# Optimization experiments

Hardware: AMD Instinct MI355X
Metric: run time of the kernel (lower is better)

## Reference

```python
import jax, jax.numpy as jnp
from jax import lax
import numpy as np

D_MODEL = 96; D_STATE = 16; SSM_RATIO = 2.0; D_CONV = 3; K = 4
D_INNER = int(SSM_RATIO * D_MODEL)      # 192
DT_RANK = -(-D_MODEL // 16)             # ceil(96/16) = 6
B_SZ = 4; H = 32; W = 32

# ---- zig-zag (snake) index helpers (static numpy) ----
def _snake_h(Hh, Ww):
    idx = np.tile(np.arange(Ww), (Hh, 1)); idx[1::2] = idx[1::2, ::-1]; return idx  # (H,W)

def _snake_v(Hh, Ww):
    idx = np.tile(np.arange(Hh)[:, None], (1, Ww)); idx[:, 1::2] = idx[::-1, 1::2]; return idx  # (H,W)

def _h_scan(x, d):
    Hh, Ww = x.shape[-2:]
    if d == 'left':
        x = jnp.flip(x, (-1, -2))
    return x[:, :, np.arange(Hh)[:, None], _snake_h(Hh, Ww)]

def _v_scan(x, d):
    Bb, Cc, Hh, Ww = x.shape
    if d == 'up':
        x = jnp.flip(x, (-1, -2))
    t = x[:, :, _snake_v(Hh, Ww), np.arange(Ww)[None, :]]  # gather along H per column
    return jnp.swapaxes(t, -1, -2).reshape(Bb, Cc, Hh, Ww)

def _h_merge(x, d):
    Hh, Ww = x.shape[-2:]
    t = x[:, :, np.arange(Hh)[:, None], _snake_h(Hh, Ww)]
    if d == 'left':
        t = jnp.flip(t, (-1, -2))
    return t

def _v_merge(x, d):
    Hh, Ww = x.shape[-2:]
    t2 = jnp.swapaxes(x, -1, -2)  # (B,C,W,H); requires H==W like the torch source
    t = t2[:, :, _snake_v(Hh, Ww), np.arange(Ww)[None, :]]
    if d == 'up':
        t = jnp.flip(t, (-1, -2))
    return t

def cross_scan(x):
    return jnp.stack([_v_scan(x, 'down'), _v_scan(x, 'up'), _h_scan(x, 'right'), _h_scan(x, 'left')], axis=1)

def cross_merge(ys):
    return (_v_merge(ys[:, 0], 'down') + _v_merge(ys[:, 1], 'up')
            + _h_merge(ys[:, 2], 'right') + _h_merge(ys[:, 3], 'left'))

def selective_scan(u, delta, A, Bs, Cs, Dp, delta_bias):
    # u,delta:(B,K,D,L)  A:(K,D,N)  Bs,Cs:(B,K,N,L)  Dp,delta_bias:(K,D)
    delta = jax.nn.softplus(delta + delta_bias[None, :, :, None])
    dA = jnp.exp(jnp.einsum('bkdl,kdn->lbkdn', delta, A))
    dBu = jnp.einsum('bkdl,bkdl,bknl->lbkdn', delta, u, Bs)
    Ct = jnp.moveaxis(Cs, -1, 0)  # (L,B,K,N)
    def step(h, inp):
        dA_t, dBu_t, c_t = inp
        h = dA_t * h + dBu_t
        return h, jnp.einsum('bkdn,bkn->bkd', h, c_t)
    h0 = jnp.zeros(dA.shape[1:], u.dtype)
    _, ys = lax.scan(step, h0, (dA, dBu, Ct))
    return jnp.moveaxis(ys, 0, -1) + Dp[None, :, :, None] * u  # (B,K,D,L)

def setup_inputs() -> dict:
    key = jax.random.key(0)
    ks = jax.random.split(key, 8)
    x = jax.random.normal(ks[0], (B_SZ, D_MODEL, H, W), jnp.float32)
    in_proj_w = jax.random.normal(ks[1], (2 * D_INNER, D_MODEL), jnp.float32) * (D_MODEL ** -0.5)
    conv_w = jax.random.normal(ks[2], (D_INNER, 1, D_CONV, D_CONV), jnp.float32) * 0.2  # depthwise
    conv_b = jnp.zeros((D_INNER,), jnp.float32)
    x_proj_w = jax.random.normal(ks[3], (K, DT_RANK + 2 * D_STATE, D_INNER), jnp.float32) * (D_INNER ** -0.5)
    s = DT_RANK ** -0.5
    dt_w = jax.random.uniform(ks[4], (K, D_INNER, DT_RANK), jnp.float32, -s, s)
    dt = jax.random.uniform(ks[5], (K, D_INNER), jnp.float32, 0.001, 0.1)
    dt_b = jnp.log(jnp.expm1(dt))  # inverse softplus, as in dt_init
    A_logs = jnp.tile(jnp.log(jnp.arange(1, D_STATE + 1, dtype=jnp.float32)), (K * D_INNER, 1))
    Ds = jnp.ones((K * D_INNER,), jnp.float32)
    gn_gamma = jnp.ones((D_INNER,), jnp.float32)
    gn_beta = jnp.zeros((D_INNER,), jnp.float32)
    out_proj_w = jax.random.normal(ks[6], (D_MODEL, D_INNER), jnp.float32) * (D_INNER ** -0.5)
    return {'x': x, 'in_proj_w': in_proj_w, 'conv_w': conv_w, 'conv_b': conv_b,
            'x_proj_w': x_proj_w, 'dt_w': dt_w, 'dt_b': dt_b, 'A_logs': A_logs, 'Ds': Ds,
            'gn_gamma': gn_gamma, 'gn_beta': gn_beta, 'out_proj_w': out_proj_w}

def reference(x, in_proj_w, conv_w, conv_b, x_proj_w, dt_w, dt_b, A_logs, Ds, gn_gamma, gn_beta, out_proj_w):
    Bb, _, Hh, Ww = x.shape; L = Hh * Ww
    xz = jnp.einsum('bchw,oc->bohw', x, in_proj_w)          # in_proj (1x1 conv, no bias)
    xx, z = jnp.split(xz, 2, axis=1)
    z = jax.nn.silu(z)
    xx = lax.conv_general_dilated(xx, conv_w, (1, 1), 'SAME', feature_group_count=D_INNER,
                                  dimension_numbers=('NCHW', 'OIHW', 'NCHW')) + conv_b[None, :, None, None]
    xx = jax.nn.silu(xx)
    xs = cross_scan(xx).reshape(Bb, K, D_INNER, L)          # 4-direction zig-zag scan
    x_dbl = jnp.einsum('bkdl,kcd->bkcl', xs, x_proj_w)
    dts = jnp.einsum('bkrl,kdr->bkdl', x_dbl[:, :, :DT_RANK], dt_w)
    Bs = x_dbl[:, :, DT_RANK:DT_RANK + D_STATE]
    Cs = x_dbl[:, :, DT_RANK + D_STATE:]
    A = -jnp.exp(A_logs).reshape(K, D_INNER, D_STATE)
    y = selective_scan(xs, dts, A, Bs, Cs, Ds.reshape(K, D_INNER), dt_b)
    y = cross_merge(y.reshape(Bb, K, D_INNER, Hh, Ww))       # (B,D,H,W)
    # out_norm: GroupNorm(1, d_inner) == layernorm over (C,H,W) per sample
    mu = jnp.mean(y, axis=(1, 2, 3), keepdims=True)
    var = jnp.var(y, axis=(1, 2, 3), keepdims=True)
    y = (y - mu) * lax.rsqrt(var + 1e-6)
    y = y * gn_gamma[None, :, None, None] + gn_beta[None, :, None, None]
    y = y * z
    return jnp.einsum('bchw,oc->bohw', y, out_proj_w)
```

## Files before the change

kernel.cpp:

```cpp
#include <hip/hip_runtime.h>
#include <math.h>

#define Bsz 4
#define DM 96
#define DI 192
#define NS 16
#define RK 6
#define KK 4
#define HH 32
#define WW 32
#define LL 1024
#define NC 32
#define CS 32

__device__ __forceinline__ float silu_f(float x) { return x / (1.f + __expf(-x)); }

__device__ __forceinline__ float2 pk_mul(float2 a, float2 b) {
    return make_float2(a.x * b.x, a.y * b.y);
}
__device__ __forceinline__ float2 pk_fma(float2 a, float2 b, float2 c) {
    return make_float2(fmaf(a.x, b.x, c.x), fmaf(a.y, b.y, c.y));
}

__device__ __forceinline__ int hw_of_l(int k, int l) {
    int a = l >> 5, r = l & 31;
    int m = (a & 1) ? 31 - r : r;
    int h, w;
    if (k < 2) { w = a; h = m; }
    else       { h = a; w = m; }
    if (k & 1) { h = 31 - h; w = 31 - w; }
    return h * 32 + w;
}

__global__ void in_proj_k(const float* __restrict__ x, const float* __restrict__ w,
                          float* __restrict__ xx, float* __restrict__ zs,
                          float* __restrict__ stats) {
    int bi = blockIdx.x;
    int t = threadIdx.x;
    if (bi == 0 && t < 2 * Bsz) stats[t] = 0.f;
    int lb = bi & 3;
    int og = (bi >> 2) % 96;
    int b = bi / 384;
    int l = lb * 256 + t;
    const float* xb = x + (size_t)b * DM * LL + l;
    float acc[4];
#pragma unroll
    for (int g = 0; g < 4; g++) acc[g] = 0.f;
    for (int c = 0; c < DM; c++) {
        float xv = xb[(size_t)c * LL];
#pragma unroll
        for (int g = 0; g < 4; g++)
            acc[g] = fmaf(xv, w[(size_t)(og * 4 + g) * DM + c], acc[g]);
    }
#pragma unroll
    for (int g = 0; g < 4; g++) {
        int o = og * 4 + g;
        if (o < DI) xx[((size_t)b * DI + o) * LL + l] = acc[g];
        else        zs[((size_t)b * DI + (o - DI)) * LL + l] = silu_f(acc[g]);
    }
}

__global__ void convT_k(const float* __restrict__ xx, const float* __restrict__ cw,
                        const float* __restrict__ cb, float* __restrict__ xxT) {
    __shared__ float tile[32][33];
    int bi = blockIdx.x;
    int h0 = bi % 32;
    int dt = (bi / 32) % 6;
    int b = bi / 192;
    int d0 = dt * 32;
    int t = threadIdx.x;
    int wi = t & 31, dg = t >> 5;

#pragma unroll
    for (int pass = 0; pass < 4; pass++) {
        int di = pass * 8 + dg;
        int d = d0 + di;
        const float* xp = xx + ((size_t)b * DI + d) * LL;
        const float* wp = cw + d * 9;
        float acc = cb[d];
#pragma unroll
        for (int kh = 0; kh < 3; kh++) {
            int hh = h0 + kh - 1;
            if (hh < 0 || hh >= HH) continue;
#pragma unroll
            for (int kw = 0; kw < 3; kw++) {
                int ww2 = wi + kw - 1;
                if (ww2 < 0 || ww2 >= WW) continue;
                acc = fmaf(xp[hh * WW + ww2], wp[kh * 3 + kw], acc);
            }
        }
        tile[wi][di] = silu_f(acc);
    }
    __syncthreads();

    int di = t & 31, w8 = t >> 5;
#pragma unroll
    for (int rep = 0; rep < 4; rep++) {
        int w2 = rep * 8 + w8;
        xxT[((size_t)b * LL + h0 * 32 + w2) * DI + d0 + di] = tile[w2][di];
    }
}

__global__ void __launch_bounds__(512)
xdbl_k(const float* __restrict__ xxT, const float* __restrict__ xpw,
       float* __restrict__ xdbl) {
    __shared__ float tile[64 * 193];
    int blk = blockIdx.x;
    int bk = blk >> 4, lt = blk & 15;
    int k = bk & 3, b = bk >> 2;
    int t = threadIdx.x;

    const float* xb = xxT + (size_t)b * LL * DI;
#pragma unroll
    for (int i = 0; i < 6; i++) {
        int j4 = t + i * 512;
        int lr = j4 / 48;
        int d4 = j4 % 48;
        int hw = hw_of_l(k, lt * 64 + lr);
        float4 v = ((const float4*)(xb + (size_t)hw * DI))[d4];
        float* dst = &tile[lr * 193 + d4 * 4];
        dst[0] = v.x; dst[1] = v.y; dst[2] = v.z; dst[3] = v.w;
    }
    __syncthreads();

    int ll = t & 63;
    int cg = t >> 6;
    int c0 = cg * 5;
    int wlim = (c0 + 5 <= 38) ? 5 : (38 - c0);
    const float* wk = xpw + (size_t)k * 38 * DI;

    float acc[5];
#pragma unroll
    for (int j = 0; j < 5; j++) acc[j] = 0.f;
    const float* xrow = &tile[ll * 193];
#pragma unroll 4
    for (int d = 0; d < DI; d++) {
        float xv = xrow[d];
#pragma unroll
        for (int j = 0; j < 5; j++) {
            int cc = c0 + j; cc = (cc > 37) ? 37 : cc;
            acc[j] = fmaf(xv, wk[(size_t)cc * DI + d], acc[j]);
        }
    }
    float* orow = xdbl + ((size_t)bk * LL + lt * 64 + ll) * 38;
#pragma unroll
    for (int j = 0; j < 5; j++)
        if (j < wlim) orow[c0 + j] = acc[j];
}

#define XDP 40

__global__ void scan_p1(const float* __restrict__ xxT, const float* __restrict__ xdbl,
                        const float* __restrict__ dtw_g, const float* __restrict__ dtb_g,
                        const float* __restrict__ Alog,
                        float* __restrict__ Pst, float* __restrict__ Hloc) {
    __shared__ float u_tile[CS * 192];
    __shared__ float xd_tile[CS * XDP];
    int blk = blockIdx.x;
    int bk = blk / NC, c = blk % NC;
    int k = bk & 3, b = bk >> 2;
    int t = threadIdx.x;

    const float* xb = xxT + (size_t)b * LL * DI;
#pragma unroll
    for (int i = 0; i < 8; i++) {
        int j4 = t + i * 192;
        int s = j4 / 48, d4 = j4 % 48;
        int hw = hw_of_l(k, c * CS + s);
        float4 v = ((const float4*)(xb + (size_t)hw * DI))[d4];
        ((float4*)(&u_tile[s * 192]))[d4] = v;
    }
    const float* xdsrc = xdbl + ((size_t)bk * LL + c * CS) * 38;
    for (int i = t; i < CS * 38; i += 192) {
        int s = i / 38, j = i - s * 38;
        int pj = (j < 6) ? 32 + j : j - 6;
        xd_tile[s * XDP + pj] = xdsrc[i];
    }
    __syncthreads();

    int d = t;
    int kd = k * DI + d;
    float A0 = -__expf(Alog[(size_t)kd * NS]);
    bool pw = true;
#pragma unroll
    for (int n = 1; n < NS; n++) {
        float An = -__expf(Alog[(size_t)kd * NS + n]);
        pw = pw && (fabsf(An - (float)(n + 1) * A0) <= 1e-4f * (float)(n + 1));
    }
    float dtw[RK];
#pragma unroll
    for (int r = 0; r < RK; r++) dtw[r] = dtw_g[(size_t)kd * RK + r];
    float dtb = dtb_g[kd];

    float2 h2[8], P2[8];
#pragma unroll
    for (int i = 0; i < 8; i++) h2[i] = make_float2(0.f, 0.f);

    if (pw) {
        float R = 1.f;
        for (int s = 0; s < CS; s++) {
            const float2* xr2 = (const float2*)(&xd_tile[s * XDP]);
            float2 bb2[8];
#pragma unroll
            for (int i = 0; i < 8; i++) bb2[i] = xr2[i];
            float2 qa = xr2[16], qb = xr2[17], qc = xr2[18];
            float dt = dtb;
            dt = fmaf(qa.x, dtw[0], dt); dt = fmaf(qa.y, dtw[1], dt);
            dt = fmaf(qb.x, dtw[2], dt); dt = fmaf(qb.y, dtw[3], dt);
            dt = fmaf(qc.x, dtw[4], dt); dt = fmaf(qc.y, dtw[5], dt);
            dt = (dt > 20.f) ? dt : __logf(1.f + __expf(dt));
            float du = dt * u_tile[s * 192 + d];
            float r1 = __expf(dt * A0);
            float r2 = r1 * r1, r4 = r2 * r2, r8 = r4 * r4;
            float2 r2v = make_float2(r2, r2), r4v = make_float2(r4, r4),
                   r8v = make_float2(r8, r8);
            float2 aa2[8];
            aa2[0] = make_float2(r1, r2);
            aa2[1] = pk_mul(aa2[0], r2v);
            aa2[2] = pk_mul(aa2[0], r4v);
            aa2[3] = pk_mul(aa2[1], r4v);
#pragma unroll
            for (int i = 0; i < 4; i++) aa2[i + 4] = pk_mul(aa2[i], r8v);
            float2 du2 = make_float2(du, du);
#pragma unroll
            for (int i = 0; i < 8; i++)
                h2[i] = pk_fma(aa2[i], h2[i], pk_mul(du2, bb2[i]));
            R *= r1;
        }
        float R2 = R * R, R4 = R2 * R2, R8 = R4 * R4;
        float2 R2v = make_float2(R2, R2), R4v = make_float2(R4, R4),
               R8v = make_float2(R8, R8);
        P2[0] = make_float2(R, R2);
        P2[1] = pk_mul(P2[0], R2v);
        P2[2] = pk_mul(P2[0], R4v);
        P2[3] = pk_mul(P2[1], R4v);
#pragma unroll
        for (int i = 0; i < 4; i++) P2[i + 4] = pk_mul(P2[i], R8v);
    } else {
        float A[NS];
#pragma unroll
        for (int n = 0; n < NS; n++) A[n] = -__expf(Alog[(size_t)kd * NS + n]);
#pragma unroll
        for (int i = 0; i < 8; i++) P2[i] = make_float2(1.f, 1.f);
        for (int s = 0; s < CS; s++) {
            const float2* xr2 = (const float2*)(&xd_tile[s * XDP]);
            float2 bb2[8];
#pragma unroll
            for (int i = 0; i < 8; i++) bb2[i] = xr2[i];
            float2 qa = xr2[16], qb = xr2[17], qc = xr2[18];
            float dt = dtb;
            dt = fmaf(qa.x, dtw[0], dt); dt = fmaf(qa.y, dtw[1], dt);
            dt = fmaf(qb.x, dtw[2], dt); dt = fmaf(qb.y, dtw[3], dt);
            dt = fmaf(qc.x, dtw[4], dt); dt = fmaf(qc.y, dtw[5], dt);
            dt = (dt > 20.f) ? dt : __logf(1.f + __expf(dt));
            float du = dt * u_tile[s * 192 + d];
            float2 du2 = make_float2(du, du);
#pragma unroll
            for (int i = 0; i < 8; i++) {
                float2 a2 = make_float2(__expf(dt * A[2 * i]),
                                        __expf(dt * A[2 * i + 1]));
                h2[i] = pk_fma(a2, h2[i], pk_mul(du2, bb2[i]));
                P2[i] = pk_mul(P2[i], a2);
            }
        }
    }
    if (c < NC - 1) {
        size_t base = ((size_t)blk * DI + d) * NS;
        float2* Pp = (float2*)(&Pst[base]);
        float2* Hp = (float2*)(&Hloc[base]);
#pragma unroll
        for (int i = 0; i < 8; i++) { Pp[i] = P2[i]; Hp[i] = h2[i]; }
    }
}

__global__ void scan_mid(const float* __restrict__ Pst, float* __restrict__ Hloc) {
    int gid = blockIdx.x * 256 + threadIdx.x;
    int bk = gid / 1536;
    int j = gid % 1536;
    const float2* Pp = (const float2*)(Pst + (size_t)bk * NC * (DI * NS)) + j;
    float2* Hp = (float2*)(Hloc + (size_t)bk * NC * (DI * NS)) + j;
    const int S = (DI * NS) / 2;

    float2 h = make_float2(0.f, 0.f);
    float2 P[4], L[4];
#pragma unroll
    for (int q = 0; q < 4; q++) { P[q] = Pp[(size_t)q * S]; L[q] = Hp[(size_t)q * S]; }
    for (int c = 0; c < NC; c += 4) {
        float2 Pn[4], Ln[4];
        if (c + 4 < NC) {
#pragma unroll
            for (int q = 0; q < 4; q++) {
                Pn[q] = Pp[(size_t)(c + 4 + q) * S];
                Ln[q] = Hp[(size_t)(c + 4 + q) * S];
            }
        }
#pragma unroll
        for (int q = 0; q < 4; q++) {
            Hp[(size_t)(c + q) * S] = h;
            h.x = fmaf(P[q].x, h.x, L[q].x);
            h.y = fmaf(P[q].y, h.y, L[q].y);
        }
#pragma unroll
        for (int q = 0; q < 4; q++) { P[q] = Pn[q]; L[q] = Ln[q]; }
    }
}

__global__ void scan_p3(const float* __restrict__ xxT, const float* __restrict__ xdbl,
                        const float* __restrict__ dtw_g, const float* __restrict__ dtb_g,
                        const float* __restrict__ Alog, const float* __restrict__ Ds,
                        const float* __restrict__ Hin, float* __restrict__ ysm) {
    __shared__ float u_tile[CS * 192];
    __shared__ float xd_tile[CS * XDP];
    int blk = blockIdx.x;
    int bk = blk / NC, c = blk % NC;
    int k = bk & 3, b = bk >> 2;
    int t = threadIdx.x;

    const float* xb = xxT + (size_t)b * LL * DI;
#pragma unroll
    for (int i = 0; i < 8; i++) {
        int j4 = t + i * 192;
        int s = j4 / 48, d4 = j4 % 48;
        int hw = hw_of_l(k, c * CS + s);
        float4 v = ((const float4*)(xb + (size_t)hw * DI))[d4];
        ((float4*)(&u_tile[s * 192]))[d4] = v;
    }
    const float* xdsrc = xdbl + ((size_t)bk * LL + c * CS) * 38;
    for (int i = t; i < CS * 38; i += 192) {
        int s = i / 38, j = i - s * 38;
        int pj = (j < 6) ? 32 + j : j - 6;
        xd_tile[s * XDP + pj] = xdsrc[i];
    }
    __syncthreads();

    int d = t;
    int kd = k * DI + d;
    float A0 = -__expf(Alog[(size_t)kd * NS]);
    bool pw = true;
#pragma unroll
    for (int n = 1; n < NS; n++) {
        float An = -__expf(Alog[(size_t)kd * NS + n]);
        pw = pw && (fabsf(An - (float)(n + 1) * A0) <= 1e-4f * (float)(n + 1));
    }
    float dtw[RK];
#pragma unroll
    for (int r = 0; r < RK; r++) dtw[r] = dtw_g[(size_t)kd * RK + r];
    float dtb = dtb_g[kd];
    float Dp = Ds[kd];

    float2 h2[8];
    size_t hbase = ((size_t)blk * DI + d) * NS;
    const float2* Hp = (const float2*)(&Hin[hbase]);
#pragma unroll
    for (int i = 0; i < 8; i++) h2[i] = Hp[i];

    float* yk = ysm + (size_t)bk * LL * DI;

    if (pw) {
        for (int s = 0; s < CS; s++) {
            const float2* xr2 = (const float2*)(&xd_tile[s * XDP]);
            float2 bb2[8], cf2[8];
#pragma unroll
            for (int i = 0; i < 8; i++) { bb2[i] = xr2[i]; cf2[i] = xr2[8 + i]; }
            float2 qa = xr2[16], qb = xr2[17], qc = xr2[18];
            float dt = dtb;
            dt = fmaf(qa.x, dtw[0], dt); dt = fmaf(qa.y, dtw[1], dt);
            dt = fmaf(qb.x, dtw[2], dt); dt = fmaf(qb.y, dtw[3], dt);
            dt = fmaf(qc.x, dtw[4], dt); dt = fmaf(qc.y, dtw[5], dt);
            dt = (dt > 20.f) ? dt : __logf(1.f + __expf(dt));
            float u = u_tile[s * 192 + d];
            float du = dt * u;
            float r1 = __expf(dt * A0);
            float r2 = r1 * r1, r4 = r2 * r2, r8 = r4 * r4;
            float2 r2v = make_float2(r2, r2), r4v = make_float2(r4, r4),
                   r8v = make_float2(r8, r8);
            float2 aa2[8];
            aa2[0] = make_float2(r1, r2);
            aa2[1] = pk_mul(aa2[0], r2v);
            aa2[2] = pk_mul(aa2[0], r4v);
            aa2[3] = pk_mul(aa2[1], r4v);
#pragma unroll
            for (int i = 0; i < 4; i++) aa2[i + 4] = pk_mul(aa2[i], r8v);
            float2 du2 = make_float2(du, du);
            float2 y2 = make_float2(0.f, 0.f);
#pragma unroll
            for (int i = 0; i < 8; i++) {
                h2[i] = pk_fma(aa2[i], h2[i], pk_mul(du2, bb2[i]));
                y2 = pk_fma(h2[i], cf2[i], y2);
            }
            int hw = hw_of_l(k, c * CS + s);
            yk[(size_t)hw * DI + d] = fmaf(Dp, u, y2.x + y2.y);
        }
    } else {
        float A[NS];
#pragma unroll
        for (int n = 0; n < NS; n++) A[n] = -__expf(Alog[(size_t)kd * NS + n]);
        for (int s = 0; s < CS; s++) {
            const float2* xr2 = (const float2*)(&xd_tile[s * XDP]);
            float2 bb2[8], cf2[8];
#pragma unroll
            for (int i = 0; i < 8; i++) { bb2[i] = xr2[i]; cf2[i] = xr2[8 + i]; }
            float2 qa = xr2[16], qb = xr2[17], qc = xr2[18];
            float dt = dtb;
            dt = fmaf(qa.x, dtw[0], dt); dt = fmaf(qa.y, dtw[1], dt);
            dt = fmaf(qb.x, dtw[2], dt); dt = fmaf(qb.y, dtw[3], dt);
            dt = fmaf(qc.x, dtw[4], dt); dt = fmaf(qc.y, dtw[5], dt);
            dt = (dt > 20.f) ? dt : __logf(1.f + __expf(dt));
            float u = u_tile[s * 192 + d];
            float du = dt * u;
            float2 du2 = make_float2(du, du);
            float2 y2 = make_float2(0.f, 0.f);
#pragma unroll
            for (int i = 0; i < 8; i++) {
                float2 a2 = make_float2(__expf(dt * A[2 * i]),
                                        __expf(dt * A[2 * i + 1]));
                h2[i] = pk_fma(a2, h2[i], pk_mul(du2, bb2[i]));
                y2 = pk_fma(h2[i], cf2[i], y2);
            }
            int hw = hw_of_l(k, c * CS + s);
            yk[(size_t)hw * DI + d] = fmaf(Dp, u, y2.x + y2.y);
        }
    }
}

#define MT 8
__global__ void merge_k(const float* __restrict__ ysm, float* __restrict__ ym,
                        float* __restrict__ stats) {
    __shared__ float tile[MT][DI + 1];
    __shared__ float sh1[3], sh2[3];
    int b = blockIdx.y;
    int hw0 = blockIdx.x * MT;
    int d = threadIdx.x;
    const float* yb = ysm + (size_t)b * KK * LL * DI;

    float s1 = 0.f, s2 = 0.f;
#pragma unroll
    for (int hwi = 0; hwi < MT; hwi++) {
        int hw = hw0 + hwi;
        float v = yb[((size_t)0 * LL + hw) * DI + d]
                + yb[((size_t)1 * LL + hw) * DI + d]
                + yb[((size_t)2 * LL + hw) * DI + d]
                + yb[((size_t)3 * LL + hw) * DI + d];
        tile[hwi][d] = v;
        s1 += v; s2 = fmaf(v, v, s2);
    }
#pragma unroll
    for (int off = 32; off > 0; off >>= 1) {
        s1 += __shfl_down(s1, off);
        s2 += __shfl_down(s2, off);
    }
    int lane = threadIdx.x & 63, wid = threadIdx.x >> 6;
    if (lane == 0) { sh1[wid] = s1; sh2[wid] = s2; }
    __syncthreads();
    if (threadIdx.x == 0) {
        atomicAdd(&stats[b * 2],     sh1[0] + sh1[1] + sh1[2]);
        atomicAdd(&stats[b * 2 + 1], sh2[0] + sh2[1] + sh2[2]);
    }
#pragma unroll
    for (int rep = 0; rep < MT; rep++) {
        int j = rep * DI + threadIdx.x;
        int d2 = j >> 3;
        int hwi = j & (MT - 1);
        ym[((size_t)b * DI + d2) * LL + hw0 + hwi] = tile[hwi][d2];
    }
}

__global__ void outz_k(const float* __restrict__ ym, const float* __restrict__ zs,
                       const float* __restrict__ g, const float* __restrict__ be,
                       const float* __restrict__ stats, const float* __restrict__ wo,
                       float* __restrict__ out) {
    int bi = blockIdx.x;
    int t = threadIdx.x;
    int lb = bi & 3;
    int og = (bi >> 2) % 32;
    int b = bi / 128;
    int l = lb * 256 + t;

    const float Ninv = 1.f / (float)(DI * LL);
    float mu = stats[b * 2] * Ninv;
    float var = stats[b * 2 + 1] * Ninv - mu * mu;
    float rstd = rsqrtf(var + 1e-6f);

    const float* yb = ym + (size_t)b * DI * LL + l;
    const float* zb = zs + (size_t)b * DI * LL + l;
    float acc[3];
#pragma unroll
    for (int gg = 0; gg < 3; gg++) acc[gg] = 0.f;
    for (int c = 0; c < DI; c++) {
        float v = (yb[(size_t)c * LL] - mu) * rstd * g[c] + be[c];
        float yv = v * zb[(size_t)c * LL];
#pragma unroll
        for (int gg = 0; gg < 3; gg++)
            acc[gg] = fmaf(yv, wo[(size_t)(og * 3 + gg) * DI + c], acc[gg]);
    }
#pragma unroll
    for (int gg = 0; gg < 3; gg++)
        out[((size_t)b * DM + og * 3 + gg) * LL + l] = acc[gg];
}

extern "C" void kernel_launch(void* const* d_in, const int* in_sizes, int n_in,
                              void* d_out, int out_size, void* d_ws, size_t ws_size,
                              hipStream_t stream) {
    const float* x    = (const float*)d_in[0];
    const float* ipw  = (const float*)d_in[1];
    const float* cw   = (const float*)d_in[2];
    const float* cb   = (const float*)d_in[3];
    const float* xpw  = (const float*)d_in[4];
    const float* dtw  = (const float*)d_in[5];
    const float* dtb  = (const float*)d_in[6];
    const float* Alog = (const float*)d_in[7];
    const float* Ds   = (const float*)d_in[8];
    const float* gng  = (const float*)d_in[9];
    const float* gnb  = (const float*)d_in[10];
    const float* opw  = (const float*)d_in[11];
    float* out = (float*)d_out;

    float* ws = (float*)d_ws;
    const size_t NPH  = (size_t)Bsz * KK * NC * DI * NS;
    const size_t o_xx   = 0;
    const size_t o_zs   = o_xx   + (size_t)Bsz * DI * LL;
    const size_t o_xxT  = o_zs   + (size_t)Bsz * DI * LL;
    const size_t o_xdbl = o_xxT  + (size_t)Bsz * LL * DI;
    const size_t o_P    = o_xdbl + (size_t)Bsz * KK * LL * 38;
    const size_t o_H    = o_P    + NPH;
    const size_t o_ysm  = o_H    + NPH;
    const size_t o_st   = o_ysm  + (size_t)Bsz * KK * LL * DI;

    float* xx    = ws + o_xx;
    float* zs    = ws + o_zs;
    float* xxT   = ws + o_xxT;
    float* xdbl  = ws + o_xdbl;
    float* Pst   = ws + o_P;
    float* Hst   = ws + o_H;
    float* ysm   = ws + o_ysm;
    float* stats = ws + o_st;
    float* ym = xx;

    hipLaunchKernelGGL(in_proj_k, dim3(1536), dim3(256), 0, stream, x, ipw, xx, zs, stats);
    hipLaunchKernelGGL(convT_k, dim3(768), dim3(256), 0, stream, xx, cw, cb, xxT);
    hipLaunchKernelGGL(xdbl_k, dim3(256), dim3(512), 0, stream, xxT, xpw, xdbl);
    hipLaunchKernelGGL(scan_p1, dim3(Bsz * KK * NC), dim3(192), 0, stream,
                       xxT, xdbl, dtw, dtb, Alog, Pst, Hst);
    hipLaunchKernelGGL(scan_mid, dim3(96), dim3(256), 0, stream, Pst, Hst);
    hipLaunchKernelGGL(scan_p3, dim3(Bsz * KK * NC), dim3(192), 0, stream,
                       xxT, xdbl, dtw, dtb, Alog, Ds, Hst, ysm);
    hipLaunchKernelGGL(merge_k, dim3(LL / MT, Bsz), dim3(192), 0, stream, ysm, ym, stats);
    hipLaunchKernelGGL(outz_k, dim3(512), dim3(256), 0, stream, ym, zs, gng, gnb, stats, opw, out);
}
```

Before: 191.4 us.

## Fold inter-chunk state propagation into scan_p3 and double chunk size

Removes the separate scan_mid kernel launch. Each scan_p3 block now recomputes its incoming state by chaining the (P, H) summaries of all preceding chunks from global memory. The chunk size doubles from 32 to 64 (16 chunks), which halves the number of blocks and cuts the serial prefix length per block. The costs are redundant prefix work in later chunks, larger shared tiles (about 59KB) that may reduce occupancy, and longer per-block serial scans with fewer blocks.

```diff
diff --git a/kernel.cpp b/kernel.cpp
--- a/kernel.cpp
+++ b/kernel.cpp
@@ -10,8 +10,8 @@
 #define HH 32
 #define WW 32
 #define LL 1024
-#define NC 32
-#define CS 32
+#define NC 16
+#define CS 64
 
 __device__ __forceinline__ float silu_f(float x) { return x / (1.f + __expf(-x)); }
 
@@ -163,7 +163,7 @@
 
     const float* xb = xxT + (size_t)b * LL * DI;
 #pragma unroll
-    for (int i = 0; i < 8; i++) {
+    for (int i = 0; i < 16; i++) {
         int j4 = t + i * 192;
         int s = j4 / 48, d4 = j4 % 48;
         int hw = hw_of_l(k, c * CS + s);
@@ -273,42 +273,11 @@
     }
 }
 
-__global__ void scan_mid(const float* __restrict__ Pst, float* __restrict__ Hloc) {
-    int gid = blockIdx.x * 256 + threadIdx.x;
-    int bk = gid / 1536;
-    int j = gid % 1536;
-    const float2* Pp = (const float2*)(Pst + (size_t)bk * NC * (DI * NS)) + j;
-    float2* Hp = (float2*)(Hloc + (size_t)bk * NC * (DI * NS)) + j;
-    const int S = (DI * NS) / 2;
-
-    float2 h = make_float2(0.f, 0.f);
-    float2 P[4], L[4];
-#pragma unroll
-    for (int q = 0; q < 4; q++) { P[q] = Pp[(size_t)q * S]; L[q] = Hp[(size_t)q * S]; }
-    for (int c = 0; c < NC; c += 4) {
-        float2 Pn[4], Ln[4];
-        if (c + 4 < NC) {
-#pragma unroll
-            for (int q = 0; q < 4; q++) {
-                Pn[q] = Pp[(size_t)(c + 4 + q) * S];
-                Ln[q] = Hp[(size_t)(c + 4 + q) * S];
-            }
-        }
-#pragma unroll
-        for (int q = 0; q < 4; q++) {
-            Hp[(size_t)(c + q) * S] = h;
-            h.x = fmaf(P[q].x, h.x, L[q].x);
-            h.y = fmaf(P[q].y, h.y, L[q].y);
-        }
-#pragma unroll
-        for (int q = 0; q < 4; q++) { P[q] = Pn[q]; L[q] = Ln[q]; }
-    }
-}
-
 __global__ void scan_p3(const float* __restrict__ xxT, const float* __restrict__ xdbl,
                         const float* __restrict__ dtw_g, const float* __restrict__ dtb_g,
                         const float* __restrict__ Alog, const float* __restrict__ Ds,
-                        const float* __restrict__ Hin, float* __restrict__ ysm) {
+                        const float* __restrict__ Pst, const float* __restrict__ Hloc,
+                        float* __restrict__ ysm) {
     __shared__ float u_tile[CS * 192];
     __shared__ float xd_tile[CS * XDP];
     int blk = blockIdx.x;
@@ -318,7 +287,7 @@
 
     const float* xb = xxT + (size_t)b * LL * DI;
 #pragma unroll
-    for (int i = 0; i < 8; i++) {
+    for (int i = 0; i < 16; i++) {
         int j4 = t + i * 192;
         int s = j4 / 48, d4 = j4 % 48;
         int hw = hw_of_l(k, c * CS + s);
@@ -349,10 +318,16 @@
     float Dp = Ds[kd];
 
     float2 h2[8];
-    size_t hbase = ((size_t)blk * DI + d) * NS;
-    const float2* Hp = (const float2*)(&Hin[hbase]);
-#pragma unroll
-    for (int i = 0; i < 8; i++) h2[i] = Hp[i];
+#pragma unroll
+    for (int i = 0; i < 8; i++) h2[i] = make_float2(0.f, 0.f);
+    for (int cc = 0; cc < c; cc++) {
+        size_t qb = (((size_t)(bk * NC + cc)) * DI + d) * NS;
+        const float2* Pq = (const float2*)(&Pst[qb]);
+        const float2* Hq = (const float2*)(&Hloc[qb]);
+#pragma unroll
+        for (int i = 0; i < 8; i++)
+            h2[i] = pk_fma(Pq[i], h2[i], Hq[i]);
+    }
 
     float* yk = ysm + (size_t)bk * LL * DI;
 
@@ -541,9 +516,8 @@
     hipLaunchKernelGGL(xdbl_k, dim3(256), dim3(512), 0, stream, xxT, xpw, xdbl);
     hipLaunchKernelGGL(scan_p1, dim3(Bsz * KK * NC), dim3(192), 0, stream,
                        xxT, xdbl, dtw, dtb, Alog, Pst, Hst);
-    hipLaunchKernelGGL(scan_mid, dim3(96), dim3(256), 0, stream, Pst, Hst);
     hipLaunchKernelGGL(scan_p3, dim3(Bsz * KK * NC), dim3(192), 0, stream,
-                       xxT, xdbl, dtw, dtb, Alog, Ds, Hst, ysm);
+                       xxT, xdbl, dtw, dtb, Alog, Ds, Pst, Hst, ysm);
     hipLaunchKernelGGL(merge_k, dim3(LL / MT, Bsz), dim3(192), 0, stream, ysm, ym, stats);
     hipLaunchKernelGGL(outz_k, dim3(512), dim3(256), 0, stream, ym, zs, gng, gnb, stats, opw, out);
 }
```

After: 199.7 us. +4.3%, slower.

## Split scan state dimension across two thread halves per channel

Applied to the files above, without the earlier changes.

Both chunked scan kernels now use 384 threads per block, and each channel's 16 state entries are split between two threads that hold 8 entries each. This halves the serial per-thread work and register load and doubles the number of wavefronts available to hide latency. In exchange, the partial outputs are written to a workspace twice as large, and merge_k must read and sum 8 partial buffers instead of 4, which adds memory traffic. The dt/softplus/exp computation is also repeated in both halves.

```diff
diff --git a/kernel.cpp b/kernel.cpp
--- a/kernel.cpp
+++ b/kernel.cpp
@@ -150,10 +150,11 @@
 
 #define XDP 40
 
-__global__ void scan_p1(const float* __restrict__ xxT, const float* __restrict__ xdbl,
-                        const float* __restrict__ dtw_g, const float* __restrict__ dtb_g,
-                        const float* __restrict__ Alog,
-                        float* __restrict__ Pst, float* __restrict__ Hloc) {
+__global__ void __launch_bounds__(384)
+scan_p1(const float* __restrict__ xxT, const float* __restrict__ xdbl,
+        const float* __restrict__ dtw_g, const float* __restrict__ dtb_g,
+        const float* __restrict__ Alog,
+        float* __restrict__ Pst, float* __restrict__ Hloc) {
     __shared__ float u_tile[CS * 192];
     __shared__ float xd_tile[CS * XDP];
     int blk = blockIdx.x;
@@ -163,22 +164,23 @@
 
     const float* xb = xxT + (size_t)b * LL * DI;
 #pragma unroll
-    for (int i = 0; i < 8; i++) {
-        int j4 = t + i * 192;
+    for (int i = 0; i < 4; i++) {
+        int j4 = t + i * 384;
         int s = j4 / 48, d4 = j4 % 48;
         int hw = hw_of_l(k, c * CS + s);
         float4 v = ((const float4*)(xb + (size_t)hw * DI))[d4];
         ((float4*)(&u_tile[s * 192]))[d4] = v;
     }
     const float* xdsrc = xdbl + ((size_t)bk * LL + c * CS) * 38;
-    for (int i = t; i < CS * 38; i += 192) {
+    for (int i = t; i < CS * 38; i += 384) {
         int s = i / 38, j = i - s * 38;
         int pj = (j < 6) ? 32 + j : j - 6;
         xd_tile[s * XDP + pj] = xdsrc[i];
     }
     __syncthreads();
 
-    int d = t;
+    int hi = (t >= 192) ? 1 : 0;
+    int d = t - hi * 192;
     int kd = k * DI + d;
     float A0 = -__expf(Alog[(size_t)kd * NS]);
     bool pw = true;
@@ -192,17 +194,17 @@
     for (int r = 0; r < RK; r++) dtw[r] = dtw_g[(size_t)kd * RK + r];
     float dtb = dtb_g[kd];
 
-    float2 h2[8], P2[8];
-#pragma unroll
-    for (int i = 0; i < 8; i++) h2[i] = make_float2(0.f, 0.f);
+    float2 h2[4], P2[4];
+#pragma unroll
+    for (int i = 0; i < 4; i++) h2[i] = make_float2(0.f, 0.f);
 
     if (pw) {
         float R = 1.f;
         for (int s = 0; s < CS; s++) {
             const float2* xr2 = (const float2*)(&xd_tile[s * XDP]);
-            float2 bb2[8];
-#pragma unroll
-            for (int i = 0; i < 8; i++) bb2[i] = xr2[i];
+            float2 bb2[4];
+#pragma unroll
+            for (int i = 0; i < 4; i++) bb2[i] = xr2[4 * hi + i];
             float2 qa = xr2[16], qb = xr2[17], qc = xr2[18];
             float dt = dtb;
             dt = fmaf(qa.x, dtw[0], dt); dt = fmaf(qa.y, dtw[1], dt);
@@ -212,41 +214,46 @@
             float du = dt * u_tile[s * 192 + d];
             float r1 = __expf(dt * A0);
             float r2 = r1 * r1, r4 = r2 * r2, r8 = r4 * r4;
-            float2 r2v = make_float2(r2, r2), r4v = make_float2(r4, r4),
-                   r8v = make_float2(r8, r8);
-            float2 aa2[8];
+            float2 r2v = make_float2(r2, r2), r4v = make_float2(r4, r4);
+            float2 aa2[4];
             aa2[0] = make_float2(r1, r2);
             aa2[1] = pk_mul(aa2[0], r2v);
             aa2[2] = pk_mul(aa2[0], r4v);
             aa2[3] = pk_mul(aa2[1], r4v);
-#pragma unroll
-            for (int i = 0; i < 4; i++) aa2[i + 4] = pk_mul(aa2[i], r8v);
+            if (hi) {
+                float2 r8v = make_float2(r8, r8);
+#pragma unroll
+                for (int i = 0; i < 4; i++) aa2[i] = pk_mul(aa2[i], r8v);
+            }
             float2 du2 = make_float2(du, du);
 #pragma unroll
-            for (int i = 0; i < 8; i++)
+            for (int i = 0; i < 4; i++)
                 h2[i] = pk_fma(aa2[i], h2[i], pk_mul(du2, bb2[i]));
             R *= r1;
         }
         float R2 = R * R, R4 = R2 * R2, R8 = R4 * R4;
-        float2 R2v = make_float2(R2, R2), R4v = make_float2(R4, R4),
-               R8v = make_float2(R8, R8);
+        float2 R2v = make_float2(R2, R2), R4v = make_float2(R4, R4);
         P2[0] = make_float2(R, R2);
         P2[1] = pk_mul(P2[0], R2v);
         P2[2] = pk_mul(P2[0], R4v);
         P2[3] = pk_mul(P2[1], R4v);
-#pragma unroll
-        for (int i = 0; i < 4; i++) P2[i + 4] = pk_mul(P2[i], R8v);
+        if (hi) {
+            float2 R8v = make_float2(R8, R8);
+#pragma unroll
+            for (int i = 0; i < 4; i++) P2[i] = pk_mul(P2[i], R8v);
+        }
     } else {
-        float A[NS];
-#pragma unroll
-        for (int n = 0; n < NS; n++) A[n] = -__expf(Alog[(size_t)kd * NS + n]);
-#pragma unroll
-        for (int i = 0; i < 8; i++) P2[i] = make_float2(1.f, 1.f);
+        float A8[8];
+#pragma unroll
+        for (int j = 0; j < 8; j++)
+            A8[j] = -__expf(Alog[(size_t)kd * NS + 8 * hi + j]);
+#pragma unroll
+        for (int i = 0; i < 4; i++) P2[i] = make_float2(1.f, 1.f);
         for (int s = 0; s < CS; s++) {
             const float2* xr2 = (const float2*)(&xd_tile[s * XDP]);
-            float2 bb2[8];
-#pragma unroll
-            for (int i = 0; i < 8; i++) bb2[i] = xr2[i];
+            float2 bb2[4];
+#pragma unroll
+            for (int i = 0; i < 4; i++) bb2[i] = xr2[4 * hi + i];
             float2 qa = xr2[16], qb = xr2[17], qc = xr2[18];
             float dt = dtb;
             dt = fmaf(qa.x, dtw[0], dt); dt = fmaf(qa.y, dtw[1], dt);
@@ -256,20 +263,20 @@
             float du = dt * u_tile[s * 192 + d];
             float2 du2 = make_float2(du, du);
 #pragma unroll
-            for (int i = 0; i < 8; i++) {
-                float2 a2 = make_float2(__expf(dt * A[2 * i]),
-                                        __expf(dt * A[2 * i + 1]));
+            for (int i = 0; i < 4; i++) {
+                float2 a2 = make_float2(__expf(dt * A8[2 * i]),
+                                        __expf(dt * A8[2 * i + 1]));
                 h2[i] = pk_fma(a2, h2[i], pk_mul(du2, bb2[i]));
                 P2[i] = pk_mul(P2[i], a2);
             }
         }
     }
     if (c < NC - 1) {
-        size_t base = ((size_t)blk * DI + d) * NS;
+        size_t base = ((size_t)blk * DI + d) * NS + 8 * hi;
         float2* Pp = (float2*)(&Pst[base]);
         float2* Hp = (float2*)(&Hloc[base]);
 #pragma unroll
-        for (int i = 0; i < 8; i++) { Pp[i] = P2[i]; Hp[i] = h2[i]; }
+        for (int i = 0; i < 4; i++) { Pp[i] = P2[i]; Hp[i] = h2[i]; }
     }
 }
 
@@ -305,10 +312,11 @@
     }
 }
 
-__global__ void scan_p3(const float* __restrict__ xxT, const float* __restrict__ xdbl,
-                        const float* __restrict__ dtw_g, const float* __restrict__ dtb_g,
-                        const float* __restrict__ Alog, const float* __restrict__ Ds,
-                        const float* __restrict__ Hin, float* __restrict__ ysm) {
+__global__ void __launch_bounds__(384)
+scan_p3(const float* __restrict__ xxT, const float* __restrict__ xdbl,
+        const float* __restrict__ dtw_g, const float* __restrict__ dtb_g,
+        const float* __restrict__ Alog, const float* __restrict__ Ds,
+        const float* __restrict__ Hin, float* __restrict__ ysm) {
     __shared__ float u_tile[CS * 192];
     __shared__ float xd_tile[CS * XDP];
     int blk = blockIdx.x;
@@ -318,22 +326,23 @@
 
     const float* xb = xxT + (size_t)b * LL * DI;
 #pragma unroll
-    for (int i = 0; i < 8; i++) {
-        int j4 = t + i * 192;
+    for (int i = 0; i < 4; i++) {
+        int j4 = t + i * 384;
         int s = j4 / 48, d4 = j4 % 48;
         int hw = hw_of_l(k, c * CS + s);
         float4 v = ((const float4*)(xb + (size_t)hw * DI))[d4];
         ((float4*)(&u_tile[s * 192]))[d4] = v;
     }
     const float* xdsrc = xdbl + ((size_t)bk * LL + c * CS) * 38;
-    for (int i = t; i < CS * 38; i += 192) {
+    for (int i = t; i < CS * 38; i += 384) {
         int s = i / 38, j = i - s * 38;
         int pj = (j < 6) ? 32 + j : j - 6;
         xd_tile[s * XDP + pj] = xdsrc[i];
     }
     __syncthreads();
 
-    int d = t;
+    int hi = (t >= 192) ? 1 : 0;
+    int d = t - hi * 192;
     int kd = k * DI + d;
     float A0 = -__expf(Alog[(size_t)kd * NS]);
     bool pw = true;
@@ -348,20 +357,23 @@
     float dtb = dtb_g[kd];
     float Dp = Ds[kd];
 
-    float2 h2[8];
-    size_t hbase = ((size_t)blk * DI + d) * NS;
+    float2 h2[4];
+    size_t hbase = ((size_t)blk * DI + d) * NS + 8 * hi;
     const float2* Hp = (const float2*)(&Hin[hbase]);
 #pragma unroll
-    for (int i = 0; i < 8; i++) h2[i] = Hp[i];
-
-    float* yk = ysm + (size_t)bk * LL * DI;
+    for (int i = 0; i < 4; i++) h2[i] = Hp[i];
+
+    float* yk = ysm + (((size_t)bk * 2 + hi) * LL) * DI;
 
     if (pw) {
         for (int s = 0; s < CS; s++) {
             const float2* xr2 = (const float2*)(&xd_tile[s * XDP]);
-            float2 bb2[8], cf2[8];
-#pragma unroll
-            for (int i = 0; i < 8; i++) { bb2[i] = xr2[i]; cf2[i] = xr2[8 + i]; }
+            float2 bb2[4], cf2[4];
+#pragma unroll
+            for (int i = 0; i < 4; i++) {
+                bb2[i] = xr2[4 * hi + i];
+                cf2[i] = xr2[8 + 4 * hi + i];
+            }
             float2 qa = xr2[16], qb = xr2[17], qc = xr2[18];
             float dt = dtb;
             dt = fmaf(qa.x, dtw[0], dt); dt = fmaf(qa.y, dtw[1], dt);
@@ -372,34 +384,41 @@
             float du = dt * u;
             float r1 = __expf(dt * A0);
             float r2 = r1 * r1, r4 = r2 * r2, r8 = r4 * r4;
-            float2 r2v = make_float2(r2, r2), r4v = make_float2(r4, r4),
-                   r8v = make_float2(r8, r8);
-            float2 aa2[8];
+            float2 r2v = make_float2(r2, r2), r4v = make_float2(r4, r4);
+            float2 aa2[4];
             aa2[0] = make_float2(r1, r2);
             aa2[1] = pk_mul(aa2[0], r2v);
             aa2[2] = pk_mul(aa2[0], r4v);
             aa2[3] = pk_mul(aa2[1], r4v);
-#pragma unroll
-            for (int i = 0; i < 4; i++) aa2[i + 4] = pk_mul(aa2[i], r8v);
+            if (hi) {
+                float2 r8v = make_float2(r8, r8);
+#pragma unroll
+                for (int i = 0; i < 4; i++) aa2[i] = pk_mul(aa2[i], r8v);
+            }
             float2 du2 = make_float2(du, du);
             float2 y2 = make_float2(0.f, 0.f);
 #pragma unroll
-            for (int i = 0; i < 8; i++) {
+            for (int i = 0; i < 4; i++) {
                 h2[i] = pk_fma(aa2[i], h2[i], pk_mul(du2, bb2[i]));
                 y2 = pk_fma(h2[i], cf2[i], y2);
             }
             int hw = hw_of_l(k, c * CS + s);
-            yk[(size_t)hw * DI + d] = fmaf(Dp, u, y2.x + y2.y);
+            float val = y2.x + y2.y + (hi ? 0.f : Dp * u);
+            yk[(size_t)hw * DI + d] = val;
         }
     } else {
-        float A[NS];
-#pragma unroll
-        for (int n = 0; n < NS; n++) A[n] = -__expf(Alog[(size_t)kd * NS + n]);
+        float A8[8];
+#pragma unroll
+        for (int j = 0; j < 8; j++)
+            A8[j] = -__expf(Alog[(size_t)kd * NS + 8 * hi + j]);
         for (int s = 0; s < CS; s++) {
             const float2* xr2 = (const float2*)(&xd_tile[s * XDP]);
-            float2 bb2[8], cf2[8];
-#pragma unroll
-            for (int i = 0; i < 8; i++) { bb2[i] = xr2[i]; cf2[i] = xr2[8 + i]; }
+            float2 bb2[4], cf2[4];
+#pragma unroll
+            for (int i = 0; i < 4; i++) {
+                bb2[i] = xr2[4 * hi + i];
+                cf2[i] = xr2[8 + 4 * hi + i];
+            }
             float2 qa = xr2[16], qb = xr2[17], qc = xr2[18];
             float dt = dtb;
             dt = fmaf(qa.x, dtw[0], dt); dt = fmaf(qa.y, dtw[1], dt);
@@ -411,14 +430,15 @@
             float2 du2 = make_float2(du, du);
             float2 y2 = make_float2(0.f, 0.f);
 #pragma unroll
-            for (int i = 0; i < 8; i++) {
-                float2 a2 = make_float2(__expf(dt * A[2 * i]),
-                                        __expf(dt * A[2 * i + 1]));
+            for (int i = 0; i < 4; i++) {
+                float2 a2 = make_float2(__expf(dt * A8[2 * i]),
+                                        __expf(dt * A8[2 * i + 1]));
                 h2[i] = pk_fma(a2, h2[i], pk_mul(du2, bb2[i]));
                 y2 = pk_fma(h2[i], cf2[i], y2);
             }
             int hw = hw_of_l(k, c * CS + s);
-            yk[(size_t)hw * DI + d] = fmaf(Dp, u, y2.x + y2.y);
+            float val = y2.x + y2.y + (hi ? 0.f : Dp * u);
+            yk[(size_t)hw * DI + d] = val;
         }
     }
 }
@@ -431,16 +451,16 @@
     int b = blockIdx.y;
     int hw0 = blockIdx.x * MT;
     int d = threadIdx.x;
-    const float* yb = ysm + (size_t)b * KK * LL * DI;
+    const float* yb = ysm + (size_t)b * KK * 2 * LL * DI;
 
     float s1 = 0.f, s2 = 0.f;
 #pragma unroll
     for (int hwi = 0; hwi < MT; hwi++) {
         int hw = hw0 + hwi;
-        float v = yb[((size_t)0 * LL + hw) * DI + d]
-                + yb[((size_t)1 * LL + hw) * DI + d]
-                + yb[((size_t)2 * LL + hw) * DI + d]
-                + yb[((size_t)3 * LL + hw) * DI + d];
+        float v = 0.f;
+#pragma unroll
+        for (int j = 0; j < KK * 2; j++)
+            v += yb[((size_t)j * LL + hw) * DI + d];
         tile[hwi][d] = v;
         s1 += v; s2 = fmaf(v, v, s2);
     }
@@ -524,7 +544,7 @@
     const size_t o_P    = o_xdbl + (size_t)Bsz * KK * LL * 38;
     const size_t o_H    = o_P    + NPH;
     const size_t o_ysm  = o_H    + NPH;
-    const size_t o_st   = o_ysm  + (size_t)Bsz * KK * LL * DI;
+    const size_t o_st   = o_ysm  + (size_t)Bsz * KK * 2 * LL * DI;
 
     float* xx    = ws + o_xx;
     float* zs    = ws + o_zs;
@@ -539,10 +559,10 @@
     hipLaunchKernelGGL(in_proj_k, dim3(1536), dim3(256), 0, stream, x, ipw, xx, zs, stats);
     hipLaunchKernelGGL(convT_k, dim3(768), dim3(256), 0, stream, xx, cw, cb, xxT);
     hipLaunchKernelGGL(xdbl_k, dim3(256), dim3(512), 0, stream, xxT, xpw, xdbl);
-    hipLaunchKernelGGL(scan_p1, dim3(Bsz * KK * NC), dim3(192), 0, stream,
+    hipLaunchKernelGGL(scan_p1, dim3(Bsz * KK * NC), dim3(384), 0, stream,
                        xxT, xdbl, dtw, dtb, Alog, Pst, Hst);
     hipLaunchKernelGGL(scan_mid, dim3(96), dim3(256), 0, stream, Pst, Hst);
-    hipLaunchKernelGGL(scan_p3, dim3(Bsz * KK * NC), dim3(192), 0, stream,
+    hipLaunchKernelGGL(scan_p3, dim3(Bsz * KK * NC), dim3(384), 0, stream,
                        xxT, xdbl, dtw, dtb, Alog, Ds, Hst, ysm);
     hipLaunchKernelGGL(merge_k, dim3(LL / MT, Bsz), dim3(192), 0, stream, ysm, ym, stats);
     hipLaunchKernelGGL(outz_k, dim3(512), dim3(256), 0, stream, ym, zs, gng, gnb, stats, opw, out);
```

Measured after the change: 198.1 us. 1.03x slower.
